# Kernel optimization log

Measured on AMD Instinct MI355X. Metric: run time of the kernel, lower is better.

## Reference

```python
import jax, jax.numpy as jnp
import numpy as np

EMBED_DIM = 1024
N_HEADS = 16
HEAD_DIM = EMBED_DIM // N_HEADS


def setup_inputs() -> dict:
    key = jax.random.key(0)
    k1, k2, k3 = jax.random.split(key, 3)
    B, T, D = 2, 2048, EMBED_DIM
    x = jax.random.normal(k1, (B, T, D), dtype=jnp.float32)
    # torch nn.Linear weights: (out_features, in_features); y = x @ W.T
    scale = 1.0 / np.sqrt(D)
    qkv_w = jax.random.uniform(k2, (3 * D, D), dtype=jnp.float32, minval=-scale, maxval=scale)
    out_w = jax.random.uniform(k3, (D, D), dtype=jnp.float32, minval=-scale, maxval=scale)
    return {"x": x, "qkv_w": qkv_w, "out_w": out_w}


def reference(x, qkv_w, out_w):
    B, T, D = x.shape
    H, hd = N_HEADS, HEAD_DIM
    qkv = jnp.einsum('btd,ed->bte', x, qkv_w)  # (B,T,3D)
    qkv = qkv.reshape(B, T, 3, H, hd)
    q = jnp.transpose(qkv[:, :, 0], (0, 2, 1, 3))  # (B,H,T,hd)
    k = jnp.transpose(qkv[:, :, 1], (0, 2, 1, 3))
    v = jnp.transpose(qkv[:, :, 2], (0, 2, 1, 3))
    scores = jnp.einsum('bhtd,bhsd->bhts', q, k) / np.sqrt(hd).astype(np.float32)
    causal = jnp.tril(jnp.ones((T, T), dtype=bool))  # True = keep
    scores = jnp.where(causal[None, None], scores, -jnp.inf)
    probs = jax.nn.softmax(scores, axis=-1)
    out = jnp.einsum('bhts,bhsd->bhtd', probs, v)
    out = jnp.transpose(out, (0, 2, 1, 3)).reshape(B, T, D)
    return jnp.einsum('btd,ed->bte', out, out_w)
```

## Files before the change

kernel.cpp:

```cpp
#include <hip/hip_runtime.h>
#include <stdint.h>

typedef __bf16 bf16;
typedef __attribute__((ext_vector_type(8))) __bf16 bf16x8;
typedef __attribute__((ext_vector_type(4))) __bf16 bf16x4;
typedef __attribute__((ext_vector_type(4))) float f32x4;

#define AS1 __attribute__((address_space(1)))
#define AS3 __attribute__((address_space(3)))

__device__ __forceinline__ void async16(const void* g, void* l) {
  __builtin_amdgcn_global_load_lds((AS1 uint32_t*)(g), (AS3 uint32_t*)(l), 16, 0, 0);
}

__device__ __forceinline__ f32x4 mfma_bf16(bf16x8 a, bf16x8 b, f32x4 c) {
  return __builtin_amdgcn_mfma_f32_16x16x32_bf16(a, b, c, 0, 0, 0);
}

__device__ __forceinline__ uint32_t pack_bf16(float a, float b) {
  union { bf16 h[2]; uint32_t u; } u;
  u.h[0] = (bf16)a; u.h[1] = (bf16)b;
  return u.u;
}

__global__ __launch_bounds__(256) void cast_f32_to_bf16_kernel(
    const float* __restrict__ in, bf16* __restrict__ out) {
  const int i = (blockIdx.x * 256 + threadIdx.x) * 4;
  const float4 v = *(const float4*)(in + i);
  bf16x4 o;
  o[0] = (bf16)v.x; o[1] = (bf16)v.y; o[2] = (bf16)v.z; o[3] = (bf16)v.w;
  *(bf16x4*)(out + i) = o;
}

__global__ __launch_bounds__(256) void gemm_qkv_kernel(
    const bf16* __restrict__ A, const bf16* __restrict__ W,
    bf16* __restrict__ QK, bf16* __restrict__ VT) {
  constexpr int K = 1024;
  __shared__ __align__(16) bf16 sm[2 * 128 * 32];
  const int tid = threadIdx.x;
  const int w = tid >> 6, lane = tid & 63;
  const int m0 = blockIdx.x * 128, n0 = blockIdx.y * 128;
  const int wm = (w >> 1) * 64, wn = (w & 1) * 64;
  const int lrow = lane & 15, lk = (lane >> 4) * 8;
  f32x4 acc[4][4] = {};

  for (int k0 = 0; k0 < K; k0 += 32) {
#pragma unroll
    for (int i = 0; i < 4; ++i) {
      const int c = tid + 256 * i;
      const bf16* src = (c < 512)
          ? (A + (size_t)(m0 + (c >> 2)) * K + k0 + (c & 3) * 8)
          : (W + (size_t)(n0 + ((c - 512) >> 2)) * K + k0 + (c & 3) * 8);
      async16(src, sm + (w * 64 + i * 256) * 8);
    }
    __syncthreads();
    bf16x8 af[4], bfr[4];
#pragma unroll
    for (int mi = 0; mi < 4; ++mi)
      af[mi] = *(const bf16x8*)&sm[(wm + mi * 16 + lrow) * 32 + lk];
#pragma unroll
    for (int ni = 0; ni < 4; ++ni)
      bfr[ni] = *(const bf16x8*)&sm[128 * 32 + (wn + ni * 16 + lrow) * 32 + lk];
#pragma unroll
    for (int mi = 0; mi < 4; ++mi)
#pragma unroll
      for (int ni = 0; ni < 4; ++ni)
        acc[mi][ni] = mfma_bf16(af[mi], bfr[ni], acc[mi][ni]);
    __syncthreads();
  }

  const bool isV = (n0 >= 2048);
#pragma unroll
  for (int mi = 0; mi < 4; ++mi) {
#pragma unroll
    for (int ni = 0; ni < 4; ++ni) {
      const int n = n0 + wn + ni * 16 + lrow;
#pragma unroll
      for (int r = 0; r < 4; ++r) {
        const int m = m0 + wm + mi * 16 + (lane >> 4) * 4 + r;
        const float v = acc[mi][ni][r];
        if (!isV) {
          QK[(size_t)m * 2048 + n] = (bf16)v;
        } else {
          const int h = (n >> 6) & 15, d = n & 63;
          const int b = m >> 11, t = m & 2047;
          VT[((size_t)((b * 16 + h) * 64 + d)) * 2048 + t] = (bf16)v;
        }
      }
    }
  }
}

__global__ __launch_bounds__(256) void attn_kernel(
    const bf16* __restrict__ QK, const bf16* __restrict__ VT,
    bf16* __restrict__ AO) {
  __shared__ __align__(16) bf16 sK[2][64 * 64];
  __shared__ __align__(16) bf16 sV[2][64 * 64];
  const int bh = blockIdx.x;
  const int qt = 15 - blockIdx.y;
  const int b = bh >> 4, h = bh & 15;
  const int tid = threadIdx.x, w = tid >> 6, lane = tid & 63;
  const int q0 = qt * 128;
  const int col = lane & 15, quad = lane >> 4;
  const bf16* Qb = QK + (size_t)b * 2048 * 2048 + h * 64;
  const bf16* Kb = Qb + 1024;
  const bf16* Vb = VT + (size_t)bh * 64 * 2048;
  const float NEG_INF = -__builtin_inff();

  bf16x8 qf[2][2];
#pragma unroll
  for (int qtile = 0; qtile < 2; ++qtile)
#pragma unroll
    for (int kk = 0; kk < 2; ++kk) {
      const int qrow = q0 + w * 32 + qtile * 16 + col;
      bf16x8 v = *(const bf16x8*)(Qb + (size_t)qrow * 2048 + kk * 32 + quad * 8);
#pragma unroll
      for (int e = 0; e < 8; ++e) v[e] = (bf16)((float)v[e] * 0.125f);
      qf[qtile][kk] = v;
    }

  auto stage = [&](int buf, int s0) {
#pragma unroll
    for (int i = 0; i < 2; ++i) {
      const int L = tid + 256 * i;
      const int row = L >> 3;
      const int ch = (L & 7) ^ (row & 7);
      async16(Kb + (size_t)(s0 + row) * 2048 + ch * 8, &sK[buf][L * 8]);
    }
#pragma unroll
    for (int i = 0; i < 2; ++i) {
      const int L = tid + 256 * i;
      const int row = L >> 3;
      const int ch = (L & 7) ^ (row & 7);
      async16(Vb + (size_t)row * 2048 + s0 + ch * 8, &sV[buf][L * 8]);
    }
  };

  f32x4 accO[4][2] = {};
  float m_i[2] = {NEG_INF, NEG_INF}, l_i[2] = {0.f, 0.f};
  const int nkv = (q0 + 128) >> 6;
  const int qmaxw = q0 + w * 32 + 31;

  stage(0, 0);

  for (int kt = 0; kt < nkv; ++kt) {
    __syncthreads();
    if (kt + 1 < nkv) stage((kt + 1) & 1, (kt + 1) * 64);
    const int s0 = kt * 64;
    if (s0 > qmaxw) continue;
    const bf16* kbuf = sK[kt & 1];
    const bf16* vbuf = sV[kt & 1];

    f32x4 st[4][2] = {};
#pragma unroll
    for (int kk = 0; kk < 2; ++kk) {
      bf16x8 kf[4];
#pragma unroll
      for (int m = 0; m < 4; ++m) {
        const int row = m * 16 + col;
        kf[m] = *(const bf16x8*)&kbuf[row * 64 + (((kk * 4 + quad) ^ (row & 7)) * 8)];
      }
#pragma unroll
      for (int m = 0; m < 4; ++m)
#pragma unroll
        for (int qtile = 0; qtile < 2; ++qtile)
          st[m][qtile] = mfma_bf16(kf[m], qf[qtile][kk], st[m][qtile]);
    }

    uint32_t pk[4][2][2];
#pragma unroll
    for (int qtile = 0; qtile < 2; ++qtile) {
      const int qg = q0 + w * 32 + qtile * 16 + col;
      float mx = NEG_INF;
#pragma unroll
      for (int m = 0; m < 4; ++m)
#pragma unroll
        for (int r = 0; r < 4; ++r) {
          const int kv = s0 + m * 16 + quad * 4 + r;
          float v = st[m][qtile][r];
          v = (kv <= qg) ? v : NEG_INF;
          st[m][qtile][r] = v;
          mx = fmaxf(mx, v);
        }
      mx = fmaxf(mx, __shfl_xor(mx, 16));
      mx = fmaxf(mx, __shfl_xor(mx, 32));
      const float mn = fmaxf(m_i[qtile], mx);
      const float alpha = __expf(m_i[qtile] - mn);
      m_i[qtile] = mn;
      float rs = 0.f;
#pragma unroll
      for (int m = 0; m < 4; ++m)
#pragma unroll
        for (int r = 0; r < 4; ++r) {
          const float p = __expf(st[m][qtile][r] - mn);
          st[m][qtile][r] = p;
          rs += p;
        }
      rs += __shfl_xor(rs, 16);
      rs += __shfl_xor(rs, 32);
      l_i[qtile] = l_i[qtile] * alpha + rs;
#pragma unroll
      for (int d = 0; d < 4; ++d) accO[d][qtile] = accO[d][qtile] * alpha;
#pragma unroll
      for (int m = 0; m < 4; ++m) {
        pk[m][qtile][0] = pack_bf16(st[m][qtile][0], st[m][qtile][1]);
        pk[m][qtile][1] = pack_bf16(st[m][qtile][2], st[m][qtile][3]);
      }
    }

    const int lane0 = ((quad & 1) * 2) * 16 + col;
    const int lane1 = lane0 + 16;
    const bool hiM = (quad >> 1) != 0;
#pragma unroll
    for (int kk = 0; kk < 2; ++kk) {
      bf16x8 pf[2];
#pragma unroll
      for (int qtile = 0; qtile < 2; ++qtile) {
        const uint32_t a0 = (uint32_t)__shfl((int)pk[2 * kk][qtile][0], lane0);
        const uint32_t b0 = (uint32_t)__shfl((int)pk[2 * kk + 1][qtile][0], lane0);
        const uint32_t a1 = (uint32_t)__shfl((int)pk[2 * kk][qtile][1], lane0);
        const uint32_t b1 = (uint32_t)__shfl((int)pk[2 * kk + 1][qtile][1], lane0);
        const uint32_t a2 = (uint32_t)__shfl((int)pk[2 * kk][qtile][0], lane1);
        const uint32_t b2 = (uint32_t)__shfl((int)pk[2 * kk + 1][qtile][0], lane1);
        const uint32_t a3 = (uint32_t)__shfl((int)pk[2 * kk][qtile][1], lane1);
        const uint32_t b3 = (uint32_t)__shfl((int)pk[2 * kk + 1][qtile][1], lane1);
        union { uint32_t u[4]; bf16x8 v; } f;
        f.u[0] = hiM ? b0 : a0;
        f.u[1] = hiM ? b1 : a1;
        f.u[2] = hiM ? b2 : a2;
        f.u[3] = hiM ? b3 : a3;
        pf[qtile] = f.v;
      }
      bf16x8 vf[4];
#pragma unroll
      for (int d = 0; d < 4; ++d) {
        const int row = d * 16 + col;
        vf[d] = *(const bf16x8*)&vbuf[row * 64 + (((kk * 4 + quad) ^ (row & 7)) * 8)];
      }
#pragma unroll
      for (int d = 0; d < 4; ++d)
#pragma unroll
        for (int qtile = 0; qtile < 2; ++qtile)
          accO[d][qtile] = mfma_bf16(vf[d], pf[qtile], accO[d][qtile]);
    }
  }

  bf16* Ob = AO + (size_t)b * 2048 * 1024 + h * 64;
#pragma unroll
  for (int qtile = 0; qtile < 2; ++qtile) {
    const float inv = 1.0f / l_i[qtile];
    const int t = q0 + w * 32 + qtile * 16 + col;
#pragma unroll
    for (int d = 0; d < 4; ++d) {
      bf16x4 o;
#pragma unroll
      for (int r = 0; r < 4; ++r) o[r] = (bf16)(accO[d][qtile][r] * inv);
      *(bf16x4*)(Ob + (size_t)t * 1024 + d * 16 + quad * 4) = o;
    }
  }
}

__global__ __launch_bounds__(256) void gemm_out_kernel(
    const bf16* __restrict__ A, const bf16* __restrict__ W,
    float* __restrict__ C) {
  constexpr int K = 1024;
  __shared__ __align__(16) bf16 sm[2 * 128 * 32];
  const int tid = threadIdx.x;
  const int w = tid >> 6, lane = tid & 63;
  const int m0 = blockIdx.x * 128, n0 = blockIdx.y * 128;
  const int wm = (w >> 1) * 64, wn = (w & 1) * 64;
  const int lrow = lane & 15, lk = (lane >> 4) * 8;
  f32x4 acc[4][4] = {};

  for (int k0 = 0; k0 < K; k0 += 32) {
#pragma unroll
    for (int i = 0; i < 4; ++i) {
      const int c = tid + 256 * i;
      const bf16* src = (c < 512)
          ? (A + (size_t)(m0 + (c >> 2)) * K + k0 + (c & 3) * 8)
          : (W + (size_t)(n0 + ((c - 512) >> 2)) * K + k0 + (c & 3) * 8);
      async16(src, sm + (w * 64 + i * 256) * 8);
    }
    __syncthreads();
    bf16x8 af[4], bfr[4];
#pragma unroll
    for (int mi = 0; mi < 4; ++mi)
      af[mi] = *(const bf16x8*)&sm[(wm + mi * 16 + lrow) * 32 + lk];
#pragma unroll
    for (int ni = 0; ni < 4; ++ni)
      bfr[ni] = *(const bf16x8*)&sm[128 * 32 + (wn + ni * 16 + lrow) * 32 + lk];
#pragma unroll
    for (int mi = 0; mi < 4; ++mi)
#pragma unroll
      for (int ni = 0; ni < 4; ++ni)
        acc[mi][ni] = mfma_bf16(af[mi], bfr[ni], acc[mi][ni]);
    __syncthreads();
  }

#pragma unroll
  for (int mi = 0; mi < 4; ++mi)
#pragma unroll
    for (int ni = 0; ni < 4; ++ni) {
      const int n = n0 + wn + ni * 16 + lrow;
#pragma unroll
      for (int r = 0; r < 4; ++r) {
        const int m = m0 + wm + mi * 16 + (lane >> 4) * 4 + r;
        C[(size_t)m * 1024 + n] = acc[mi][ni][r];
      }
    }
}

extern "C" void kernel_launch(void* const* d_in, const int* in_sizes, int n_in,
                              void* d_out, int out_size, void* d_ws, size_t ws_size,
                              hipStream_t stream) {
  const float* x     = (const float*)d_in[0];
  const float* qkv_w = (const float*)d_in[1];
  const float* out_w = (const float*)d_in[2];
  float* out = (float*)d_out;

  char* ws = (char*)d_ws;
  bf16* xb    = (bf16*)(ws);
  bf16* aob   = (bf16*)(ws);
  bf16* wqkvb = (bf16*)(ws + 8u * 1024 * 1024);
  bf16* wob   = (bf16*)(ws + 14u * 1024 * 1024);
  bf16* qkb   = (bf16*)(ws + 16u * 1024 * 1024);
  bf16* vtb   = (bf16*)(ws + 32u * 1024 * 1024);

  cast_f32_to_bf16_kernel<<<4096, 256, 0, stream>>>(x, xb);
  cast_f32_to_bf16_kernel<<<3072, 256, 0, stream>>>(qkv_w, wqkvb);
  cast_f32_to_bf16_kernel<<<1024, 256, 0, stream>>>(out_w, wob);
  gemm_qkv_kernel<<<dim3(32, 24), 256, 0, stream>>>(xb, wqkvb, qkb, vtb);
  attn_kernel<<<dim3(32, 16), 256, 0, stream>>>(qkb, vtb, aob);
  gemm_out_kernel<<<dim3(32, 8), 256, 0, stream>>>(aob, wob, out);
}
```

Measured before the change: 211.9 us.

## Halve attention query tile, specialize causal masking, use exp2, fuse cast kernels

The attention kernel now gives each block 64 query rows (16 per wave) instead of 128, doubling the grid to 1024 blocks so that occupancy and load balance improve across the causal triangle. Only the diagonal KV tile applies the causal mask; off-diagonal tiles skip the compare and select. The softmax folds log2(e) into the Q scale and uses the hardware exp2. The three fp32-to-bf16 cast launches are merged into one kernel. In exchange, each block does less MFMA work per K/V tile it stages, so shared-memory staging traffic per FLOP doubles.

Measured after the change: 192.5 us. 9.1% less time.

```diff
diff --git a/kernel.cpp b/kernel.cpp
--- a/kernel.cpp
+++ b/kernel.cpp
@@ -23,13 +23,22 @@
   return u.u;
 }
 
-__global__ __launch_bounds__(256) void cast_f32_to_bf16_kernel(
-    const float* __restrict__ in, bf16* __restrict__ out) {
-  const int i = (blockIdx.x * 256 + threadIdx.x) * 4;
-  const float4 v = *(const float4*)(in + i);
+__global__ __launch_bounds__(256) void cast_all_kernel(
+    const float* __restrict__ x, const float* __restrict__ w1,
+    const float* __restrict__ w2, bf16* __restrict__ xb,
+    bf16* __restrict__ w1b, bf16* __restrict__ w2b) {
+  const int bid = blockIdx.x;
+  const float* src;
+  bf16* dst;
+  int base;
+  if (bid < 4096) { src = x;  dst = xb;  base = bid; }
+  else if (bid < 7168) { src = w1; dst = w1b; base = bid - 4096; }
+  else { src = w2; dst = w2b; base = bid - 7168; }
+  const int i = (base * 256 + threadIdx.x) * 4;
+  const float4 v = *(const float4*)(src + i);
   bf16x4 o;
   o[0] = (bf16)v.x; o[1] = (bf16)v.y; o[2] = (bf16)v.z; o[3] = (bf16)v.w;
-  *(bf16x4*)(out + i) = o;
+  *(bf16x4*)(dst + i) = o;
 }
 
 __global__ __launch_bounds__(256) void gemm_qkv_kernel(
@@ -97,27 +106,26 @@
   __shared__ __align__(16) bf16 sK[2][64 * 64];
   __shared__ __align__(16) bf16 sV[2][64 * 64];
   const int bh = blockIdx.x;
-  const int qt = 15 - blockIdx.y;
+  const int qt = 31 - blockIdx.y;
   const int b = bh >> 4, h = bh & 15;
   const int tid = threadIdx.x, w = tid >> 6, lane = tid & 63;
-  const int q0 = qt * 128;
+  const int q0 = qt * 64;
   const int col = lane & 15, quad = lane >> 4;
   const bf16* Qb = QK + (size_t)b * 2048 * 2048 + h * 64;
   const bf16* Kb = Qb + 1024;
   const bf16* Vb = VT + (size_t)bh * 64 * 2048;
   const float NEG_INF = -__builtin_inff();
-
-  bf16x8 qf[2][2];
-#pragma unroll
-  for (int qtile = 0; qtile < 2; ++qtile)
-#pragma unroll
-    for (int kk = 0; kk < 2; ++kk) {
-      const int qrow = q0 + w * 32 + qtile * 16 + col;
-      bf16x8 v = *(const bf16x8*)(Qb + (size_t)qrow * 2048 + kk * 32 + quad * 8);
-#pragma unroll
-      for (int e = 0; e < 8; ++e) v[e] = (bf16)((float)v[e] * 0.125f);
-      qf[qtile][kk] = v;
-    }
+  constexpr float QSCALE = 0.18033688011112042f;
+
+  const int qrow = q0 + w * 16 + col;
+  bf16x8 qf[2];
+#pragma unroll
+  for (int kk = 0; kk < 2; ++kk) {
+    bf16x8 v = *(const bf16x8*)(Qb + (size_t)qrow * 2048 + kk * 32 + quad * 8);
+#pragma unroll
+    for (int e = 0; e < 8; ++e) v[e] = (bf16)((float)v[e] * QSCALE);
+    qf[kk] = v;
+  }
 
   auto stage = [&](int buf, int s0) {
 #pragma unroll
@@ -136,22 +144,20 @@
     }
   };
 
-  f32x4 accO[4][2] = {};
-  float m_i[2] = {NEG_INF, NEG_INF}, l_i[2] = {0.f, 0.f};
-  const int nkv = (q0 + 128) >> 6;
-  const int qmaxw = q0 + w * 32 + 31;
+  f32x4 accO[4] = {};
+  float m_i = NEG_INF, l_i = 0.f;
+  const int lane0 = ((quad & 1) * 2) * 16 + col;
+  const int lane1 = lane0 + 16;
+  const bool hiM = (quad >> 1) != 0;
 
   stage(0, 0);
 
-  for (int kt = 0; kt < nkv; ++kt) {
-    __syncthreads();
-    if (kt + 1 < nkv) stage((kt + 1) & 1, (kt + 1) * 64);
+  auto body = [&](int kt, bool masked) {
     const int s0 = kt * 64;
-    if (s0 > qmaxw) continue;
     const bf16* kbuf = sK[kt & 1];
     const bf16* vbuf = sV[kt & 1];
 
-    f32x4 st[4][2] = {};
+    f32x4 st[4] = {};
 #pragma unroll
     for (int kk = 0; kk < 2; ++kk) {
       bf16x8 kf[4];
@@ -162,75 +168,66 @@
       }
 #pragma unroll
       for (int m = 0; m < 4; ++m)
-#pragma unroll
-        for (int qtile = 0; qtile < 2; ++qtile)
-          st[m][qtile] = mfma_bf16(kf[m], qf[qtile][kk], st[m][qtile]);
-    }
-
-    uint32_t pk[4][2][2];
-#pragma unroll
-    for (int qtile = 0; qtile < 2; ++qtile) {
-      const int qg = q0 + w * 32 + qtile * 16 + col;
-      float mx = NEG_INF;
+        st[m] = mfma_bf16(kf[m], qf[kk], st[m]);
+    }
+
+    float mx = NEG_INF;
+    if (masked) {
+      const int qg = qrow;
 #pragma unroll
       for (int m = 0; m < 4; ++m)
 #pragma unroll
         for (int r = 0; r < 4; ++r) {
           const int kv = s0 + m * 16 + quad * 4 + r;
-          float v = st[m][qtile][r];
+          float v = st[m][r];
           v = (kv <= qg) ? v : NEG_INF;
-          st[m][qtile][r] = v;
+          st[m][r] = v;
           mx = fmaxf(mx, v);
         }
-      mx = fmaxf(mx, __shfl_xor(mx, 16));
-      mx = fmaxf(mx, __shfl_xor(mx, 32));
-      const float mn = fmaxf(m_i[qtile], mx);
-      const float alpha = __expf(m_i[qtile] - mn);
-      m_i[qtile] = mn;
-      float rs = 0.f;
+    } else {
 #pragma unroll
       for (int m = 0; m < 4; ++m)
 #pragma unroll
-        for (int r = 0; r < 4; ++r) {
-          const float p = __expf(st[m][qtile][r] - mn);
-          st[m][qtile][r] = p;
-          rs += p;
-        }
-      rs += __shfl_xor(rs, 16);
-      rs += __shfl_xor(rs, 32);
-      l_i[qtile] = l_i[qtile] * alpha + rs;
-#pragma unroll
-      for (int d = 0; d < 4; ++d) accO[d][qtile] = accO[d][qtile] * alpha;
-#pragma unroll
-      for (int m = 0; m < 4; ++m) {
-        pk[m][qtile][0] = pack_bf16(st[m][qtile][0], st[m][qtile][1]);
-        pk[m][qtile][1] = pack_bf16(st[m][qtile][2], st[m][qtile][3]);
-      }
-    }
-
-    const int lane0 = ((quad & 1) * 2) * 16 + col;
-    const int lane1 = lane0 + 16;
-    const bool hiM = (quad >> 1) != 0;
+        for (int r = 0; r < 4; ++r) mx = fmaxf(mx, st[m][r]);
+    }
+    mx = fmaxf(mx, __shfl_xor(mx, 16));
+    mx = fmaxf(mx, __shfl_xor(mx, 32));
+    const float mn = fmaxf(m_i, mx);
+    const float alpha = __builtin_amdgcn_exp2f(m_i - mn);
+    m_i = mn;
+    float rs = 0.f;
+    uint32_t pk[4][2];
+#pragma unroll
+    for (int m = 0; m < 4; ++m) {
+      float p0 = __builtin_amdgcn_exp2f(st[m][0] - mn);
+      float p1 = __builtin_amdgcn_exp2f(st[m][1] - mn);
+      float p2 = __builtin_amdgcn_exp2f(st[m][2] - mn);
+      float p3 = __builtin_amdgcn_exp2f(st[m][3] - mn);
+      rs += (p0 + p1) + (p2 + p3);
+      pk[m][0] = pack_bf16(p0, p1);
+      pk[m][1] = pack_bf16(p2, p3);
+    }
+    rs += __shfl_xor(rs, 16);
+    rs += __shfl_xor(rs, 32);
+    l_i = l_i * alpha + rs;
+#pragma unroll
+    for (int d = 0; d < 4; ++d) accO[d] = accO[d] * alpha;
+
 #pragma unroll
     for (int kk = 0; kk < 2; ++kk) {
-      bf16x8 pf[2];
-#pragma unroll
-      for (int qtile = 0; qtile < 2; ++qtile) {
-        const uint32_t a0 = (uint32_t)__shfl((int)pk[2 * kk][qtile][0], lane0);
-        const uint32_t b0 = (uint32_t)__shfl((int)pk[2 * kk + 1][qtile][0], lane0);
-        const uint32_t a1 = (uint32_t)__shfl((int)pk[2 * kk][qtile][1], lane0);
-        const uint32_t b1 = (uint32_t)__shfl((int)pk[2 * kk + 1][qtile][1], lane0);
-        const uint32_t a2 = (uint32_t)__shfl((int)pk[2 * kk][qtile][0], lane1);
-        const uint32_t b2 = (uint32_t)__shfl((int)pk[2 * kk + 1][qtile][0], lane1);
-        const uint32_t a3 = (uint32_t)__shfl((int)pk[2 * kk][qtile][1], lane1);
-        const uint32_t b3 = (uint32_t)__shfl((int)pk[2 * kk + 1][qtile][1], lane1);
-        union { uint32_t u[4]; bf16x8 v; } f;
-        f.u[0] = hiM ? b0 : a0;
-        f.u[1] = hiM ? b1 : a1;
-        f.u[2] = hiM ? b2 : a2;
-        f.u[3] = hiM ? b3 : a3;
-        pf[qtile] = f.v;
-      }
+      const uint32_t a0 = (uint32_t)__shfl((int)pk[2 * kk][0], lane0);
+      const uint32_t b0 = (uint32_t)__shfl((int)pk[2 * kk + 1][0], lane0);
+      const uint32_t a1 = (uint32_t)__shfl((int)pk[2 * kk][1], lane0);
+      const uint32_t b1 = (uint32_t)__shfl((int)pk[2 * kk + 1][1], lane0);
+      const uint32_t a2 = (uint32_t)__shfl((int)pk[2 * kk][0], lane1);
+      const uint32_t b2 = (uint32_t)__shfl((int)pk[2 * kk + 1][0], lane1);
+      const uint32_t a3 = (uint32_t)__shfl((int)pk[2 * kk][1], lane1);
+      const uint32_t b3 = (uint32_t)__shfl((int)pk[2 * kk + 1][1], lane1);
+      union { uint32_t u[4]; bf16x8 v; } f;
+      f.u[0] = hiM ? b0 : a0;
+      f.u[1] = hiM ? b1 : a1;
+      f.u[2] = hiM ? b2 : a2;
+      f.u[3] = hiM ? b3 : a3;
       bf16x8 vf[4];
 #pragma unroll
       for (int d = 0; d < 4; ++d) {
@@ -239,24 +236,26 @@
       }
 #pragma unroll
       for (int d = 0; d < 4; ++d)
-#pragma unroll
-        for (int qtile = 0; qtile < 2; ++qtile)
-          accO[d][qtile] = mfma_bf16(vf[d], pf[qtile], accO[d][qtile]);
-    }
-  }
+        accO[d] = mfma_bf16(vf[d], f.v, accO[d]);
+    }
+  };
+
+  for (int kt = 0; kt < qt; ++kt) {
+    __syncthreads();
+    stage((kt + 1) & 1, (kt + 1) * 64);
+    body(kt, false);
+  }
+  __syncthreads();
+  body(qt, true);
 
   bf16* Ob = AO + (size_t)b * 2048 * 1024 + h * 64;
-#pragma unroll
-  for (int qtile = 0; qtile < 2; ++qtile) {
-    const float inv = 1.0f / l_i[qtile];
-    const int t = q0 + w * 32 + qtile * 16 + col;
-#pragma unroll
-    for (int d = 0; d < 4; ++d) {
-      bf16x4 o;
-#pragma unroll
-      for (int r = 0; r < 4; ++r) o[r] = (bf16)(accO[d][qtile][r] * inv);
-      *(bf16x4*)(Ob + (size_t)t * 1024 + d * 16 + quad * 4) = o;
-    }
+  const float inv = 1.0f / l_i;
+#pragma unroll
+  for (int d = 0; d < 4; ++d) {
+    bf16x4 o;
+#pragma unroll
+    for (int r = 0; r < 4; ++r) o[r] = (bf16)(accO[d][r] * inv);
+    *(bf16x4*)(Ob + (size_t)qrow * 1024 + d * 16 + quad * 4) = o;
   }
 }
 
@@ -326,10 +325,8 @@
   bf16* qkb   = (bf16*)(ws + 16u * 1024 * 1024);
   bf16* vtb   = (bf16*)(ws + 32u * 1024 * 1024);
 
-  cast_f32_to_bf16_kernel<<<4096, 256, 0, stream>>>(x, xb);
-  cast_f32_to_bf16_kernel<<<3072, 256, 0, stream>>>(qkv_w, wqkvb);
-  cast_f32_to_bf16_kernel<<<1024, 256, 0, stream>>>(out_w, wob);
+  cast_all_kernel<<<8192, 256, 0, stream>>>(x, qkv_w, out_w, xb, wqkvb, wob);
   gemm_qkv_kernel<<<dim3(32, 24), 256, 0, stream>>>(xb, wqkvb, qkb, vtb);
-  attn_kernel<<<dim3(32, 16), 256, 0, stream>>>(qkb, vtb, aob);
+  attn_kernel<<<dim3(32, 32), 256, 0, stream>>>(qkb, vtb, aob);
   gemm_out_kernel<<<dim3(32, 8), 256, 0, stream>>>(aob, wob, out);
 }
```
